# Optimization experiments

Measured on AMD Instinct MI355X. Metric: run time of the kernel, lower is better.

## Reference

```python
import jax, jax.numpy as jnp
import numpy as np

B, L, K, M, N, P, D = 8, 512, 512, 64, 64, 64, 64  # M == D required for residual add


def _layernorm(x, gamma, beta, eps=1e-3):  # keras LayerNormalization default eps
    mu = jnp.mean(x, axis=-1, keepdims=True)
    var = jnp.var(x, axis=-1, keepdims=True)
    return (x - mu) * jax.lax.rsqrt(var + eps) * gamma + beta


def setup_inputs() -> dict:
    key = jax.random.key(0)
    ks = jax.random.split(key, 5)
    return {
        "q": jax.random.normal(ks[0], (B, L, D), dtype=jnp.float32),
        "k": jax.random.normal(ks[1], (B, K, D), dtype=jnp.float32),
        "vq": jax.random.normal(ks[2], (B, L, M, N), dtype=jnp.float32),
        "vk": jax.random.normal(ks[3], (B, K, P, N), dtype=jnp.float32),
        "vexp": jax.random.normal(ks[4], (B, K, P), dtype=jnp.float32),
        "scale": jnp.ones((), dtype=jnp.float32),      # keras Attention use_scale param (init 1)
        "ln_gamma": jnp.ones((D,), dtype=jnp.float32),  # LayerNormalization gamma
        "ln_beta": jnp.zeros((D,), dtype=jnp.float32),  # LayerNormalization beta
    }


def reference(q, k, vq, vk, vexp, scale, ln_gamma, ln_beta):
    # scores: keras Attention with use_scale -> scale * q @ k^T  (B, L, K)
    scores = scale * jnp.einsum('bld,bkd->blk', q, k)
    # no mask in this call path; plain softmax over keys
    weights = jax.nn.softmax(scores, axis=-1)

    # Original value path (materializes 5D 'blkmp'):
    #   s1 = einsum('blmn,bkpn->blkmp', vq, vk)
    #   v  = einsum('blkmp,bkp->blkm', s1, vexp)
    #   out = einsum('blk,blkm->blm', weights, v)
    # Mathematically identical reassociation that never builds the 5D tensor:
    vkc = jnp.einsum('bkpn,bkp->bkn', vk, vexp)       # contract P first
    tmp = jnp.einsum('blk,bkn->bln', weights, vkc)    # softmax-weighted combine over K
    attn_out = jnp.einsum('blmn,bln->blm', vq, tmp)   # contract N -> (B, L, M)

    # BaseAttentionCell / CrossAttention: residual add + LayerNorm
    return _layernorm(q + attn_out, ln_gamma, ln_beta)
```

## Files before the change

### kernel.cpp

```cpp
#include <hip/hip_runtime.h>

#define BB 8
#define LL 512
#define KK 512
#define DD 64
#define TL 4

__global__ __launch_bounds__(256) void vkc_kernel(const float* __restrict__ vk,
                                                  const float* __restrict__ vexp,
                                                  float* __restrict__ vkc) {
    const int wave = (blockIdx.x << 2) + (threadIdx.x >> 6);
    const int lane = threadIdx.x & 63;

    const float ve_reg = vexp[wave * 64 + lane];
    const int n0 = (lane & 15) << 2;
    const float* base = vk + (long)wave * (64 * 64);

    float ax = 0.f, ay = 0.f, az = 0.f, aw = 0.f;
    #pragma unroll
    for (int it = 0; it < 16; ++it) {
        const int p = (lane >> 4) + (it << 2);
        const float4 v4 = *(const float4*)(base + p * 64 + n0);
        const float w = __shfl(ve_reg, p, 64);
        ax += v4.x * w; ay += v4.y * w; az += v4.z * w; aw += v4.w * w;
    }
    ax += __shfl_down(ax, 32, 64); ax += __shfl_down(ax, 16, 64);
    ay += __shfl_down(ay, 32, 64); ay += __shfl_down(ay, 16, 64);
    az += __shfl_down(az, 32, 64); az += __shfl_down(az, 16, 64);
    aw += __shfl_down(aw, 32, 64); aw += __shfl_down(aw, 16, 64);

    if ((lane & 48) == 0) {
        float4 r; r.x = ax; r.y = ay; r.z = az; r.w = aw;
        *(float4*)(vkc + wave * 64 + n0) = r;
    }
}

__global__ __launch_bounds__(256) void attn_kernel(const float* __restrict__ q,
                                                   const float* __restrict__ k,
                                                   const float* __restrict__ vq,
                                                   const float* __restrict__ vkc,
                                                   const float* __restrict__ scale_p,
                                                   const float* __restrict__ gamma,
                                                   const float* __restrict__ beta,
                                                   float* __restrict__ out) {
    __shared__ float q_s[TL * 64];
    __shared__ float sc[TL][KK];
    __shared__ float tmpp[4][TL][64];
    __shared__ float tmp_s[TL][64];
    __shared__ float attn_s[TL][64];

    const int t = threadIdx.x;
    const int wave = t >> 6;
    const int lane = t & 63;
    const int blk = blockIdx.x;
    const int batch = blk >> 7;
    const int l0 = (blk & 127) * TL;

    const float scale = scale_p[0];

    q_s[t] = q[(batch * LL + l0) * 64 + t];
    __syncthreads();

    {
        const float* kb = k + batch * KK * 64;
        const float4* q4 = (const float4*)q_s;
        #pragma unroll
        for (int it = 0; it < 2; ++it) {
            const int kk = t + it * 256;
            const float4* krow = (const float4*)(kb + kk * 64);
            float a0 = 0.f, a1 = 0.f, a2 = 0.f, a3 = 0.f;
            #pragma unroll
            for (int dc = 0; dc < 16; ++dc) {
                const float4 kv = krow[dc];
                const float4 p0 = q4[0 * 16 + dc];
                const float4 p1 = q4[1 * 16 + dc];
                const float4 p2 = q4[2 * 16 + dc];
                const float4 p3 = q4[3 * 16 + dc];
                a0 += p0.x * kv.x + p0.y * kv.y + p0.z * kv.z + p0.w * kv.w;
                a1 += p1.x * kv.x + p1.y * kv.y + p1.z * kv.z + p1.w * kv.w;
                a2 += p2.x * kv.x + p2.y * kv.y + p2.z * kv.z + p2.w * kv.w;
                a3 += p3.x * kv.x + p3.y * kv.y + p3.z * kv.z + p3.w * kv.w;
            }
            sc[0][kk] = scale * a0;
            sc[1][kk] = scale * a1;
            sc[2][kk] = scale * a2;
            sc[3][kk] = scale * a3;
        }
    }
    __syncthreads();

    {
        float v[8];
        float mx = -1e30f;
        #pragma unroll
        for (int j = 0; j < 8; ++j) {
            v[j] = sc[wave][lane + 64 * j];
            mx = fmaxf(mx, v[j]);
        }
        #pragma unroll
        for (int off = 32; off; off >>= 1) mx = fmaxf(mx, __shfl_xor(mx, off, 64));
        float s = 0.f;
        #pragma unroll
        for (int j = 0; j < 8; ++j) { v[j] = __expf(v[j] - mx); s += v[j]; }
        #pragma unroll
        for (int off = 32; off; off >>= 1) s += __shfl_xor(s, off, 64);
        const float inv = 1.0f / s;
        #pragma unroll
        for (int j = 0; j < 8; ++j) sc[wave][lane + 64 * j] = v[j] * inv;
    }
    __syncthreads();

    {
        const float* vkcb = vkc + batch * KK * 64;
        float a0 = 0.f, a1 = 0.f, a2 = 0.f, a3 = 0.f;
        const int kbeg = wave * 128;
        for (int kk = kbeg; kk < kbeg + 128; ++kk) {
            const float vv = vkcb[kk * 64 + lane];
            a0 += sc[0][kk] * vv;
            a1 += sc[1][kk] * vv;
            a2 += sc[2][kk] * vv;
            a3 += sc[3][kk] * vv;
        }
        tmpp[wave][0][lane] = a0;
        tmpp[wave][1][lane] = a1;
        tmpp[wave][2][lane] = a2;
        tmpp[wave][3][lane] = a3;
    }
    __syncthreads();
    {
        tmp_s[wave][lane] = tmpp[0][wave][lane] + tmpp[1][wave][lane] +
                            tmpp[2][wave][lane] + tmpp[3][wave][lane];
    }
    __syncthreads();

    {
        const float* vql = vq + (long)(batch * LL + l0 + wave) * 4096;
        const int n0 = (lane & 15) << 2;
        const float4 t4 = *(const float4*)&tmp_s[wave][n0];
        #pragma unroll
        for (int it = 0; it < 16; ++it) {
            const int flat = it * 256 + lane * 4;
            const float4 v4 = *(const float4*)(vql + flat);
            float part = v4.x * t4.x + v4.y * t4.y + v4.z * t4.z + v4.w * t4.w;
            part += __shfl_down(part, 8, 16);
            part += __shfl_down(part, 4, 16);
            part += __shfl_down(part, 2, 16);
            part += __shfl_down(part, 1, 16);
            if ((lane & 15) == 0) attn_s[wave][it * 4 + (lane >> 4)] = part;
        }
    }

    {
        const float x = q_s[wave * 64 + lane] + attn_s[wave][lane];
        float s1 = x, s2 = x * x;
        #pragma unroll
        for (int off = 32; off; off >>= 1) {
            s1 += __shfl_xor(s1, off, 64);
            s2 += __shfl_xor(s2, off, 64);
        }
        const float mean = s1 * (1.0f / 64.0f);
        const float var = s2 * (1.0f / 64.0f) - mean * mean;
        const float r = rsqrtf(var + 1e-3f);
        const float y = (x - mean) * r * gamma[lane] + beta[lane];
        out[(batch * LL + l0 + wave) * 64 + lane] = y;
    }
}

extern "C" void kernel_launch(void* const* d_in, const int* in_sizes, int n_in,
                              void* d_out, int out_size, void* d_ws, size_t ws_size,
                              hipStream_t stream) {
    const float* q     = (const float*)d_in[0];
    const float* k     = (const float*)d_in[1];
    const float* vq    = (const float*)d_in[2];
    const float* vk    = (const float*)d_in[3];
    const float* vexp  = (const float*)d_in[4];
    const float* scale = (const float*)d_in[5];
    const float* gamma = (const float*)d_in[6];
    const float* beta  = (const float*)d_in[7];
    float* out = (float*)d_out;
    float* vkc = (float*)d_ws;

    vkc_kernel<<<1024, 256, 0, stream>>>(vk, vexp, vkc);
    attn_kernel<<<1024, 256, 0, stream>>>(q, k, vq, vkc, scale, gamma, beta, out);
}
```

Measured before the change: 206.5 us.

## Overlap vkc reduction with score softmax in one launch, split post stage

Merges the vk·vexp contraction and the QK^T plus softmax into one launch with interleaved block types, so the score work no longer waits on vkc and the two can overlap. The normalized weights go to a workspace buffer. A second kernel with 128-thread blocks of two rows prefetches vq into registers before the weighted vkc sum and LayerNorm. This adds an 8 MB weights round trip through global memory and needs enough workspace, otherwise it falls back to the old path.

```diff
diff --git a/kernel.cpp b/kernel.cpp
--- a/kernel.cpp
+++ b/kernel.cpp
@@ -1,81 +1,63 @@
 #include <hip/hip_runtime.h>
 
-#define BB 8
-#define LL 512
-#define KK 512
-#define DD 64
-#define TL 4
-
-__global__ __launch_bounds__(256) void vkc_kernel(const float* __restrict__ vk,
-                                                  const float* __restrict__ vexp,
-                                                  float* __restrict__ vkc) {
-    const int wave = (blockIdx.x << 2) + (threadIdx.x >> 6);
-    const int lane = threadIdx.x & 63;
-
-    const float ve_reg = vexp[wave * 64 + lane];
-    const int n0 = (lane & 15) << 2;
-    const float* base = vk + (long)wave * (64 * 64);
-
-    float ax = 0.f, ay = 0.f, az = 0.f, aw = 0.f;
-    #pragma unroll
-    for (int it = 0; it < 16; ++it) {
-        const int p = (lane >> 4) + (it << 2);
-        const float4 v4 = *(const float4*)(base + p * 64 + n0);
-        const float w = __shfl(ve_reg, p, 64);
-        ax += v4.x * w; ay += v4.y * w; az += v4.z * w; aw += v4.w * w;
-    }
-    ax += __shfl_down(ax, 32, 64); ax += __shfl_down(ax, 16, 64);
-    ay += __shfl_down(ay, 32, 64); ay += __shfl_down(ay, 16, 64);
-    az += __shfl_down(az, 32, 64); az += __shfl_down(az, 16, 64);
-    aw += __shfl_down(aw, 32, 64); aw += __shfl_down(aw, 16, 64);
-
-    if ((lane & 48) == 0) {
-        float4 r; r.x = ax; r.y = ay; r.z = az; r.w = aw;
-        *(float4*)(vkc + wave * 64 + n0) = r;
-    }
-}
-
-__global__ __launch_bounds__(256) void attn_kernel(const float* __restrict__ q,
-                                                   const float* __restrict__ k,
-                                                   const float* __restrict__ vq,
-                                                   const float* __restrict__ vkc,
-                                                   const float* __restrict__ scale_p,
-                                                   const float* __restrict__ gamma,
-                                                   const float* __restrict__ beta,
-                                                   float* __restrict__ out) {
-    __shared__ float q_s[TL * 64];
-    __shared__ float sc[TL][KK];
-    __shared__ float tmpp[4][TL][64];
-    __shared__ float tmp_s[TL][64];
-    __shared__ float attn_s[TL][64];
-
+
+__global__ __launch_bounds__(256) void fused_pre(const float* __restrict__ q,
+                                                 const float* __restrict__ k,
+                                                 const float* __restrict__ vk,
+                                                 const float* __restrict__ vexp,
+                                                 const float* __restrict__ scale_p,
+                                                 float* __restrict__ vkc,
+                                                 float* __restrict__ wts) {
     const int t = threadIdx.x;
-    const int wave = t >> 6;
-    const int lane = t & 63;
-    const int blk = blockIdx.x;
-    const int batch = blk >> 7;
-    const int l0 = (blk & 127) * TL;
-
-    const float scale = scale_p[0];
-
-    q_s[t] = q[(batch * LL + l0) * 64 + t];
-    __syncthreads();
-
-    {
-        const float* kb = k + batch * KK * 64;
+    const int wv = t >> 6, lane = t & 63;
+    const int type = (gridDim.x > 1024) ? (blockIdx.x & 1) : 0;
+    const int id   = (gridDim.x > 1024) ? (blockIdx.x >> 1) : blockIdx.x;
+
+    if (type == 0) {
+        const int row = (id << 2) + wv;
+        const float ve = vexp[row * 64 + lane];
+        const int n0 = (lane & 15) << 2;
+        const int p0 = lane >> 4;
+        const float* base = vk + (long)row * 4096;
+        float4 v[16];
+        #pragma unroll
+        for (int it = 0; it < 16; ++it)
+            v[it] = *(const float4*)(base + (p0 + (it << 2)) * 64 + n0);
+        float ax = 0.f, ay = 0.f, az = 0.f, aw = 0.f;
+        #pragma unroll
+        for (int it = 0; it < 16; ++it) {
+            const float w = __shfl(ve, p0 + (it << 2), 64);
+            ax += v[it].x * w; ay += v[it].y * w; az += v[it].z * w; aw += v[it].w * w;
+        }
+        ax += __shfl_down(ax, 32, 64); ax += __shfl_down(ax, 16, 64);
+        ay += __shfl_down(ay, 32, 64); ay += __shfl_down(ay, 16, 64);
+        az += __shfl_down(az, 32, 64); az += __shfl_down(az, 16, 64);
+        aw += __shfl_down(aw, 32, 64); aw += __shfl_down(aw, 16, 64);
+        if ((lane & 48) == 0) {
+            float4 r; r.x = ax; r.y = ay; r.z = az; r.w = aw;
+            *(float4*)(vkc + row * 64 + n0) = r;
+        }
+    } else {
+        __shared__ float q_s[256];
+        __shared__ float sc[4][512];
+        const int batch = id >> 7;
+        const int l0 = (id & 127) << 2;
+        const float scale = scale_p[0];
+
+        q_s[t] = q[(batch * 512 + l0) * 64 + t];
+        __syncthreads();
+
+        const float* kb = k + batch * 512 * 64;
         const float4* q4 = (const float4*)q_s;
         #pragma unroll
         for (int it = 0; it < 2; ++it) {
-            const int kk = t + it * 256;
+            const int kk = t + (it << 8);
             const float4* krow = (const float4*)(kb + kk * 64);
             float a0 = 0.f, a1 = 0.f, a2 = 0.f, a3 = 0.f;
             #pragma unroll
             for (int dc = 0; dc < 16; ++dc) {
                 const float4 kv = krow[dc];
-                const float4 p0 = q4[0 * 16 + dc];
-                const float4 p1 = q4[1 * 16 + dc];
-                const float4 p2 = q4[2 * 16 + dc];
-                const float4 p3 = q4[3 * 16 + dc];
+                const float4 p0 = q4[dc], p1 = q4[16 + dc], p2 = q4[32 + dc], p3 = q4[48 + dc];
                 a0 += p0.x * kv.x + p0.y * kv.y + p0.z * kv.z + p0.w * kv.w;
                 a1 += p1.x * kv.x + p1.y * kv.y + p1.z * kv.z + p1.w * kv.w;
                 a2 += p2.x * kv.x + p2.y * kv.y + p2.z * kv.z + p2.w * kv.w;
@@ -86,17 +68,11 @@
             sc[2][kk] = scale * a2;
             sc[3][kk] = scale * a3;
         }
-    }
-    __syncthreads();
-
-    {
-        float v[8];
-        float mx = -1e30f;
-        #pragma unroll
-        for (int j = 0; j < 8; ++j) {
-            v[j] = sc[wave][lane + 64 * j];
-            mx = fmaxf(mx, v[j]);
-        }
+        __syncthreads();
+
+        float v[8]; float mx = -1e30f;
+        #pragma unroll
+        for (int j = 0; j < 8; ++j) { v[j] = sc[wv][lane + 64 * j]; mx = fmaxf(mx, v[j]); }
         #pragma unroll
         for (int off = 32; off; off >>= 1) mx = fmaxf(mx, __shfl_xor(mx, off, 64));
         float s = 0.f;
@@ -105,42 +81,157 @@
         #pragma unroll
         for (int off = 32; off; off >>= 1) s += __shfl_xor(s, off, 64);
         const float inv = 1.0f / s;
+        float* wrow = wts + (batch * 512 + l0 + wv) * 512;
+        #pragma unroll
+        for (int j = 0; j < 8; ++j) wrow[lane + 64 * j] = v[j] * inv;
+    }
+}
+
+__global__ __launch_bounds__(128) void fused_post(const float* __restrict__ q,
+                                                  const float* __restrict__ vq,
+                                                  const float* __restrict__ vkc,
+                                                  const float* __restrict__ wts,
+                                                  const float* __restrict__ gamma,
+                                                  const float* __restrict__ beta,
+                                                  float* __restrict__ out) {
+    __shared__ float w_s[2 * 512];
+    __shared__ float tp[2][2][64];
+    __shared__ float tmp_s[2][64];
+    __shared__ float attn_s[2][64];
+
+    const int t = threadIdx.x, wv = t >> 6, lane = t & 63;
+    const int batch = blockIdx.x >> 8;
+    const int l0 = (blockIdx.x & 255) << 1;
+    const int row = batch * 512 + l0 + wv;
+
+    const float* vql = vq + (long)row * 4096;
+    float4 v[16];
+    #pragma unroll
+    for (int it = 0; it < 16; ++it)
+        v[it] = *(const float4*)(vql + it * 256 + lane * 4);
+    const float qreg = q[row * 64 + lane];
+
+    const float* wg = wts + (batch * 512 + l0) * 512;
+    #pragma unroll
+    for (int i = 0; i < 2; ++i)
+        *(float4*)(w_s + t * 4 + i * 512) = *(const float4*)(wg + t * 4 + i * 512);
+    __syncthreads();
+
+    const float* vkcb = vkc + batch * 512 * 64;
+    float a0 = 0.f, a1 = 0.f;
+    const int kbeg = wv << 8;
+    #pragma unroll 16
+    for (int kk = kbeg; kk < kbeg + 256; ++kk) {
+        const float vv = vkcb[kk * 64 + lane];
+        a0 += w_s[kk] * vv;
+        a1 += w_s[512 + kk] * vv;
+    }
+    tp[wv][0][lane] = a0; tp[wv][1][lane] = a1;
+    __syncthreads();
+    tmp_s[wv][lane] = tp[0][wv][lane] + tp[1][wv][lane];
+
+    const int n0 = (lane & 15) << 2;
+    const float4 t4 = *(const float4*)&tmp_s[wv][n0];
+    #pragma unroll
+    for (int it = 0; it < 16; ++it) {
+        float part = v[it].x * t4.x + v[it].y * t4.y + v[it].z * t4.z + v[it].w * t4.w;
+        part += __shfl_down(part, 8, 16);
+        part += __shfl_down(part, 4, 16);
+        part += __shfl_down(part, 2, 16);
+        part += __shfl_down(part, 1, 16);
+        if ((lane & 15) == 0) attn_s[wv][it * 4 + (lane >> 4)] = part;
+    }
+
+    const float x = qreg + attn_s[wv][lane];
+    float s1 = x, s2 = x * x;
+    #pragma unroll
+    for (int off = 32; off; off >>= 1) {
+        s1 += __shfl_xor(s1, off, 64);
+        s2 += __shfl_xor(s2, off, 64);
+    }
+    const float mean = s1 * (1.0f / 64.0f);
+    const float var = s2 * (1.0f / 64.0f) - mean * mean;
+    const float r = rsqrtf(var + 1e-3f);
+    out[row * 64 + lane] = (x - mean) * r * gamma[lane] + beta[lane];
+}
+
+__global__ __launch_bounds__(256) void attn_fallback(const float* __restrict__ q,
+                                                     const float* __restrict__ k,
+                                                     const float* __restrict__ vq,
+                                                     const float* __restrict__ vkc,
+                                                     const float* __restrict__ scale_p,
+                                                     const float* __restrict__ gamma,
+                                                     const float* __restrict__ beta,
+                                                     float* __restrict__ out) {
+    __shared__ float q_s[256];
+    __shared__ float sc[4][512];
+    __shared__ float tmpp[4][4][64];
+    __shared__ float tmp_s[4][64];
+    __shared__ float attn_s[4][64];
+    const int t = threadIdx.x, wave = t >> 6, lane = t & 63;
+    const int batch = blockIdx.x >> 7, l0 = (blockIdx.x & 127) * 4;
+    const float scale = scale_p[0];
+    q_s[t] = q[(batch * 512 + l0) * 64 + t];
+    __syncthreads();
+    {
+        const float* kb = k + batch * 512 * 64;
+        const float4* q4 = (const float4*)q_s;
+        for (int it = 0; it < 2; ++it) {
+            const int kk = t + it * 256;
+            const float4* krow = (const float4*)(kb + kk * 64);
+            float a0 = 0.f, a1 = 0.f, a2 = 0.f, a3 = 0.f;
+            #pragma unroll
+            for (int dc = 0; dc < 16; ++dc) {
+                const float4 kv = krow[dc];
+                const float4 p0 = q4[dc], p1 = q4[16 + dc], p2 = q4[32 + dc], p3 = q4[48 + dc];
+                a0 += p0.x * kv.x + p0.y * kv.y + p0.z * kv.z + p0.w * kv.w;
+                a1 += p1.x * kv.x + p1.y * kv.y + p1.z * kv.z + p1.w * kv.w;
+                a2 += p2.x * kv.x + p2.y * kv.y + p2.z * kv.z + p2.w * kv.w;
+                a3 += p3.x * kv.x + p3.y * kv.y + p3.z * kv.z + p3.w * kv.w;
+            }
+            sc[0][kk] = scale * a0; sc[1][kk] = scale * a1;
+            sc[2][kk] = scale * a2; sc[3][kk] = scale * a3;
+        }
+    }
+    __syncthreads();
+    {
+        float v[8]; float mx = -1e30f;
+        #pragma unroll
+        for (int j = 0; j < 8; ++j) { v[j] = sc[wave][lane + 64 * j]; mx = fmaxf(mx, v[j]); }
+        #pragma unroll
+        for (int off = 32; off; off >>= 1) mx = fmaxf(mx, __shfl_xor(mx, off, 64));
+        float s = 0.f;
+        #pragma unroll
+        for (int j = 0; j < 8; ++j) { v[j] = __expf(v[j] - mx); s += v[j]; }
+        #pragma unroll
+        for (int off = 32; off; off >>= 1) s += __shfl_xor(s, off, 64);
+        const float inv = 1.0f / s;
         #pragma unroll
         for (int j = 0; j < 8; ++j) sc[wave][lane + 64 * j] = v[j] * inv;
     }
     __syncthreads();
-
-    {
-        const float* vkcb = vkc + batch * KK * 64;
+    {
+        const float* vkcb = vkc + batch * 512 * 64;
         float a0 = 0.f, a1 = 0.f, a2 = 0.f, a3 = 0.f;
-        const int kbeg = wave * 128;
-        for (int kk = kbeg; kk < kbeg + 128; ++kk) {
+        for (int kk = wave * 128; kk < wave * 128 + 128; ++kk) {
             const float vv = vkcb[kk * 64 + lane];
-            a0 += sc[0][kk] * vv;
-            a1 += sc[1][kk] * vv;
-            a2 += sc[2][kk] * vv;
-            a3 += sc[3][kk] * vv;
-        }
-        tmpp[wave][0][lane] = a0;
-        tmpp[wave][1][lane] = a1;
-        tmpp[wave][2][lane] = a2;
-        tmpp[wave][3][lane] = a3;
-    }
-    __syncthreads();
-    {
-        tmp_s[wave][lane] = tmpp[0][wave][lane] + tmpp[1][wave][lane] +
-                            tmpp[2][wave][lane] + tmpp[3][wave][lane];
-    }
-    __syncthreads();
-
-    {
-        const float* vql = vq + (long)(batch * LL + l0 + wave) * 4096;
+            a0 += sc[0][kk] * vv; a1 += sc[1][kk] * vv;
+            a2 += sc[2][kk] * vv; a3 += sc[3][kk] * vv;
+        }
+        tmpp[wave][0][lane] = a0; tmpp[wave][1][lane] = a1;
+        tmpp[wave][2][lane] = a2; tmpp[wave][3][lane] = a3;
+    }
+    __syncthreads();
+    tmp_s[wave][lane] = tmpp[0][wave][lane] + tmpp[1][wave][lane] +
+                        tmpp[2][wave][lane] + tmpp[3][wave][lane];
+    __syncthreads();
+    {
+        const float* vql = vq + (long)(batch * 512 + l0 + wave) * 4096;
         const int n0 = (lane & 15) << 2;
         const float4 t4 = *(const float4*)&tmp_s[wave][n0];
         #pragma unroll
         for (int it = 0; it < 16; ++it) {
-            const int flat = it * 256 + lane * 4;
-            const float4 v4 = *(const float4*)(vql + flat);
+            const float4 v4 = *(const float4*)(vql + it * 256 + lane * 4);
             float part = v4.x * t4.x + v4.y * t4.y + v4.z * t4.z + v4.w * t4.w;
             part += __shfl_down(part, 8, 16);
             part += __shfl_down(part, 4, 16);
@@ -149,20 +240,15 @@
             if ((lane & 15) == 0) attn_s[wave][it * 4 + (lane >> 4)] = part;
         }
     }
-
     {
         const float x = q_s[wave * 64 + lane] + attn_s[wave][lane];
         float s1 = x, s2 = x * x;
         #pragma unroll
-        for (int off = 32; off; off >>= 1) {
-            s1 += __shfl_xor(s1, off, 64);
-            s2 += __shfl_xor(s2, off, 64);
-        }
+        for (int off = 32; off; off >>= 1) { s1 += __shfl_xor(s1, off, 64); s2 += __shfl_xor(s2, off, 64); }
         const float mean = s1 * (1.0f / 64.0f);
         const float var = s2 * (1.0f / 64.0f) - mean * mean;
         const float r = rsqrtf(var + 1e-3f);
-        const float y = (x - mean) * r * gamma[lane] + beta[lane];
-        out[(batch * LL + l0 + wave) * 64 + lane] = y;
+        out[(batch * 512 + l0 + wave) * 64 + lane] = (x - mean) * r * gamma[lane] + beta[lane];
     }
 }
 
@@ -178,8 +264,16 @@
     const float* gamma = (const float*)d_in[6];
     const float* beta  = (const float*)d_in[7];
     float* out = (float*)d_out;
+
     float* vkc = (float*)d_ws;
-
-    vkc_kernel<<<1024, 256, 0, stream>>>(vk, vexp, vkc);
-    attn_kernel<<<1024, 256, 0, stream>>>(q, k, vq, vkc, scale, gamma, beta, out);
-}
+    const size_t need = (size_t)(8 * 512 * 64 + 8 * 512 * 512) * sizeof(float);
+
+    if (ws_size >= need) {
+        float* wts = vkc + 8 * 512 * 64;
+        fused_pre<<<2048, 256, 0, stream>>>(q, k, vk, vexp, scale, vkc, wts);
+        fused_post<<<2048, 128, 0, stream>>>(q, vq, vkc, wts, gamma, beta, out);
+    } else {
+        fused_pre<<<1024, 256, 0, stream>>>(q, k, vk, vexp, scale, vkc, nullptr);
+        attn_fallback<<<1024, 256, 0, stream>>>(q, k, vq, vkc, scale, gamma, beta, out);
+    }
+}
```

Result: slower. 324.5 us (+57.2%).

## Halve query rows per block, double grid, vectorize weighted vkc combine

Applied to the files above, without the earlier changes.

The attention kernel now handles two query rows per block instead of four, which doubles the grid to 2048 blocks. The softmax-weighted combine over keys now uses float4 loads with a cross-lane shuffle reduction instead of scalar loads. The vq contraction is split across two waves per row. The aim is more parallelism and better memory access per wave. The cost is that each block reads K and vkc for only two rows, so K and vkc traffic doubles, and half the waves sit idle during softmax and layernorm.

```diff
diff --git a/kernel.cpp b/kernel.cpp
--- a/kernel.cpp
+++ b/kernel.cpp
@@ -1,10 +1,5 @@
 #include <hip/hip_runtime.h>
 
-#define BB 8
-#define LL 512
-#define KK 512
-#define DD 64
-#define TL 4
 
 __global__ __launch_bounds__(256) void vkc_kernel(const float* __restrict__ vk,
                                                   const float* __restrict__ vexp,
@@ -14,7 +9,7 @@
 
     const float ve_reg = vexp[wave * 64 + lane];
     const int n0 = (lane & 15) << 2;
-    const float* base = vk + (long)wave * (64 * 64);
+    const float* base = vk + (long)wave * 4096;
 
     float ax = 0.f, ay = 0.f, az = 0.f, aw = 0.f;
     #pragma unroll
@@ -43,60 +38,49 @@
                                                    const float* __restrict__ gamma,
                                                    const float* __restrict__ beta,
                                                    float* __restrict__ out) {
-    __shared__ float q_s[TL * 64];
-    __shared__ float sc[TL][KK];
-    __shared__ float tmpp[4][TL][64];
-    __shared__ float tmp_s[TL][64];
-    __shared__ float attn_s[TL][64];
+    __shared__ float q_s[2 * 64];
+    __shared__ float sc[2][512];
+    __shared__ float tp[4][2][64];
+    __shared__ float tmp_s[2][64];
+    __shared__ float attn_s[2][64];
 
     const int t = threadIdx.x;
-    const int wave = t >> 6;
+    const int wv = t >> 6;
     const int lane = t & 63;
-    const int blk = blockIdx.x;
-    const int batch = blk >> 7;
-    const int l0 = (blk & 127) * TL;
+    const int batch = blockIdx.x >> 8;
+    const int l0 = (blockIdx.x & 255) << 1;
 
     const float scale = scale_p[0];
 
-    q_s[t] = q[(batch * LL + l0) * 64 + t];
+    if (t < 128) q_s[t] = q[(batch * 512 + l0) * 64 + t];
     __syncthreads();
 
     {
-        const float* kb = k + batch * KK * 64;
+        const float* kb = k + batch * 512 * 64;
         const float4* q4 = (const float4*)q_s;
         #pragma unroll
-        for (int it = 0; it < 2; ++it) {
-            const int kk = t + it * 256;
+        for (int rep = 0; rep < 2; ++rep) {
+            const int kk = t + (rep << 8);
             const float4* krow = (const float4*)(kb + kk * 64);
-            float a0 = 0.f, a1 = 0.f, a2 = 0.f, a3 = 0.f;
+            float a0 = 0.f, a1 = 0.f;
             #pragma unroll
             for (int dc = 0; dc < 16; ++dc) {
                 const float4 kv = krow[dc];
-                const float4 p0 = q4[0 * 16 + dc];
-                const float4 p1 = q4[1 * 16 + dc];
-                const float4 p2 = q4[2 * 16 + dc];
-                const float4 p3 = q4[3 * 16 + dc];
+                const float4 p0 = q4[dc];
+                const float4 p1 = q4[16 + dc];
                 a0 += p0.x * kv.x + p0.y * kv.y + p0.z * kv.z + p0.w * kv.w;
                 a1 += p1.x * kv.x + p1.y * kv.y + p1.z * kv.z + p1.w * kv.w;
-                a2 += p2.x * kv.x + p2.y * kv.y + p2.z * kv.z + p2.w * kv.w;
-                a3 += p3.x * kv.x + p3.y * kv.y + p3.z * kv.z + p3.w * kv.w;
             }
             sc[0][kk] = scale * a0;
             sc[1][kk] = scale * a1;
-            sc[2][kk] = scale * a2;
-            sc[3][kk] = scale * a3;
         }
     }
     __syncthreads();
 
-    {
-        float v[8];
-        float mx = -1e30f;
+    if (wv < 2) {
+        float v[8]; float mx = -1e30f;
         #pragma unroll
-        for (int j = 0; j < 8; ++j) {
-            v[j] = sc[wave][lane + 64 * j];
-            mx = fmaxf(mx, v[j]);
-        }
+        for (int j = 0; j < 8; ++j) { v[j] = sc[wv][lane + 64 * j]; mx = fmaxf(mx, v[j]); }
         #pragma unroll
         for (int off = 32; off; off >>= 1) mx = fmaxf(mx, __shfl_xor(mx, off, 64));
         float s = 0.f;
@@ -106,52 +90,67 @@
         for (int off = 32; off; off >>= 1) s += __shfl_xor(s, off, 64);
         const float inv = 1.0f / s;
         #pragma unroll
-        for (int j = 0; j < 8; ++j) sc[wave][lane + 64 * j] = v[j] * inv;
+        for (int j = 0; j < 8; ++j) sc[wv][lane + 64 * j] = v[j] * inv;
     }
     __syncthreads();
 
     {
-        const float* vkcb = vkc + batch * KK * 64;
-        float a0 = 0.f, a1 = 0.f, a2 = 0.f, a3 = 0.f;
-        const int kbeg = wave * 128;
-        for (int kk = kbeg; kk < kbeg + 128; ++kk) {
-            const float vv = vkcb[kk * 64 + lane];
-            a0 += sc[0][kk] * vv;
-            a1 += sc[1][kk] * vv;
-            a2 += sc[2][kk] * vv;
-            a3 += sc[3][kk] * vv;
+        const float* vkcb = vkc + batch * 512 * 64;
+        const int ksub = lane >> 4;
+        const int n0 = (lane & 15) << 2;
+        float4 a0 = {0.f, 0.f, 0.f, 0.f}, a1 = {0.f, 0.f, 0.f, 0.f};
+        const int kbeg = wv << 7;
+        #pragma unroll 8
+        for (int i = 0; i < 32; ++i) {
+            const int kk = kbeg + (i << 2) + ksub;
+            const float4 v4 = *(const float4*)(vkcb + kk * 64 + n0);
+            const float w0 = sc[0][kk];
+            const float w1 = sc[1][kk];
+            a0.x += w0 * v4.x; a0.y += w0 * v4.y; a0.z += w0 * v4.z; a0.w += w0 * v4.w;
+            a1.x += w1 * v4.x; a1.y += w1 * v4.y; a1.z += w1 * v4.z; a1.w += w1 * v4.w;
         }
-        tmpp[wave][0][lane] = a0;
-        tmpp[wave][1][lane] = a1;
-        tmpp[wave][2][lane] = a2;
-        tmpp[wave][3][lane] = a3;
+        a0.x += __shfl_down(a0.x, 32, 64); a0.x += __shfl_down(a0.x, 16, 64);
+        a0.y += __shfl_down(a0.y, 32, 64); a0.y += __shfl_down(a0.y, 16, 64);
+        a0.z += __shfl_down(a0.z, 32, 64); a0.z += __shfl_down(a0.z, 16, 64);
+        a0.w += __shfl_down(a0.w, 32, 64); a0.w += __shfl_down(a0.w, 16, 64);
+        a1.x += __shfl_down(a1.x, 32, 64); a1.x += __shfl_down(a1.x, 16, 64);
+        a1.y += __shfl_down(a1.y, 32, 64); a1.y += __shfl_down(a1.y, 16, 64);
+        a1.z += __shfl_down(a1.z, 32, 64); a1.z += __shfl_down(a1.z, 16, 64);
+        a1.w += __shfl_down(a1.w, 32, 64); a1.w += __shfl_down(a1.w, 16, 64);
+        if (lane < 16) {
+            *(float4*)&tp[wv][0][lane << 2] = a0;
+            *(float4*)&tp[wv][1][lane << 2] = a1;
+        }
     }
     __syncthreads();
-    {
-        tmp_s[wave][lane] = tmpp[0][wave][lane] + tmpp[1][wave][lane] +
-                            tmpp[2][wave][lane] + tmpp[3][wave][lane];
+    if (t < 128) {
+        const int l = t >> 6, n = t & 63;
+        tmp_s[l][n] = tp[0][l][n] + tp[1][l][n] + tp[2][l][n] + tp[3][l][n];
     }
     __syncthreads();
 
     {
-        const float* vql = vq + (long)(batch * LL + l0 + wave) * 4096;
+        const int l = wv >> 1;
+        const int half = wv & 1;
+        const float* vql = vq + (long)(batch * 512 + l0 + l) * 4096;
         const int n0 = (lane & 15) << 2;
-        const float4 t4 = *(const float4*)&tmp_s[wave][n0];
+        const float4 t4 = *(const float4*)&tmp_s[l][n0];
         #pragma unroll
-        for (int it = 0; it < 16; ++it) {
-            const int flat = it * 256 + lane * 4;
-            const float4 v4 = *(const float4*)(vql + flat);
+        for (int it = 0; it < 8; ++it) {
+            const int itg = (half << 3) + it;
+            const float4 v4 = *(const float4*)(vql + itg * 256 + lane * 4);
             float part = v4.x * t4.x + v4.y * t4.y + v4.z * t4.z + v4.w * t4.w;
             part += __shfl_down(part, 8, 16);
             part += __shfl_down(part, 4, 16);
             part += __shfl_down(part, 2, 16);
             part += __shfl_down(part, 1, 16);
-            if ((lane & 15) == 0) attn_s[wave][it * 4 + (lane >> 4)] = part;
+            if ((lane & 15) == 0) attn_s[l][(itg << 2) + (lane >> 4)] = part;
         }
     }
+    __syncthreads();
 
-    {
-        const float x = q_s[wave * 64 + lane] + attn_s[wave][lane];
+    if (wv < 2) {
+        const float x = q_s[wv * 64 + lane] + attn_s[wv][lane];
         float s1 = x, s2 = x * x;
         #pragma unroll
         for (int off = 32; off; off >>= 1) {
@@ -161,8 +160,8 @@
         const float mean = s1 * (1.0f / 64.0f);
         const float var = s2 * (1.0f / 64.0f) - mean * mean;
         const float r = rsqrtf(var + 1e-3f);
-        const float y = (x - mean) * r * gamma[lane] + beta[lane];
-        out[(batch * LL + l0 + wave) * 64 + lane] = y;
+        out[(batch * 512 + l0 + wv) * 64 + lane] =
+            (x - mean) * r * gamma[lane] + beta[lane];
     }
 }
 
@@ -181,5 +180,5 @@
     float* vkc = (float*)d_ws;
 
     vkc_kernel<<<1024, 256, 0, stream>>>(vk, vexp, vkc);
-    attn_kernel<<<1024, 256, 0, stream>>>(q, k, vq, vkc, scale, gamma, beta, out);
+    attn_kernel<<<2048, 256, 0, stream>>>(q, k, vq, vkc, scale, gamma, beta, out);
 }
```

Result: slower. 231.5 us (+12.1%).
